# Optimization experiments

Hardware: AMD Instinct MI355X
Metric: run time of the kernel (lower is better)

## Reference

```python
import jax, jax.numpy as jnp
import numpy as np

# Gating config (matches init_kwargs)
N_GROUPS = 4        # n_expert_groups
TOPK_GROUPS = 2     # n_limited_groups
TOPK = 4            # n_activated_experts
ROUTE_SCALE = 1.0


def setup_inputs() -> dict:
    key = jax.random.key(0)
    ks = jax.random.split(key, 8)
    T, D, E, I = 2048, 1024, 16, 512
    s = 0.02  # init scale for sane numerics
    return {
        "x": jax.random.normal(ks[0], (T, D), jnp.float32),
        "gate_w": jax.random.normal(ks[1], (E, D), jnp.float32) * s,
        "w1": jax.random.normal(ks[2], (E, I, D), jnp.float32) * s,
        "w2": jax.random.normal(ks[3], (E, D, I), jnp.float32) * s,
        "w3": jax.random.normal(ks[4], (E, I, D), jnp.float32) * s,
        "ws1": jax.random.normal(ks[5], (I, D), jnp.float32) * s,
        "ws2": jax.random.normal(ks[6], (D, I), jnp.float32) * s,
        "ws3": jax.random.normal(ks[7], (I, D), jnp.float32) * s,
    }


def _gate(x, gate_w):
    # GateDeepSeekV3.forward: softmax scores, group-limited routing, top-k experts.
    T = x.shape[0]
    scores = jax.nn.softmax((x @ gate_w.T).astype(jnp.float32), axis=-1)  # [T, E]
    original_scores = scores
    E = scores.shape[-1]
    # group-limited routing: keep top `TOPK_GROUPS` groups by max score (bias is None)
    s = scores.reshape(T, N_GROUPS, E // N_GROUPS)
    group_scores = s.max(axis=-1)                                  # [T, G]
    _, gidx = jax.lax.top_k(group_scores, TOPK_GROUPS)             # [T, Gk]
    mask = jnp.zeros((T, N_GROUPS), scores.dtype).at[jnp.arange(T)[:, None], gidx].set(1.0)
    s = (s * mask[:, :, None]).reshape(T, E)
    _, indices = jax.lax.top_k(s, TOPK)                            # [T, topk]
    weights = jnp.take_along_axis(original_scores, indices, axis=1) * ROUTE_SCALE
    return weights.astype(x.dtype), indices


def reference(x, gate_w, w1, w2, w3, ws1, ws2, ws3):
    T, D = x.shape
    E = w1.shape[0]
    weights, indices = _gate(x, gate_w)
    # dense [T, E] combine weights (topk indices are unique per token)
    gate_dense = jnp.zeros((T, E), x.dtype).at[jnp.arange(T)[:, None], indices].add(weights)
    # routed experts: y_t = sum_e g[t,e] * W2_e (silu(W1_e x) * (W3_e x))
    h = jax.nn.silu(jnp.einsum('td,eid->tei', x, w1)) * jnp.einsum('td,eid->tei', x, w3)
    y = jnp.einsum('tei,te,edi->td', h, gate_dense, w2)
    # shared expert MLP over all tokens
    z = (jax.nn.silu(x @ ws1.T) * (x @ ws3.T)) @ ws2.T
    return y + z
```

## Files before the change

kernel.cpp:

```cpp
#include <hip/hip_runtime.h>
#include <hip/hip_bf16.h>
#include <math.h>

typedef float v4f __attribute__((ext_vector_type(4)));
typedef short v8s __attribute__((ext_vector_type(8)));

#define T_TOK   2048
#define DDIM    1024
#define NE      16
#define IDIM    512
#define S_ROUTED 8192
#define S_ALL   10240
#define MAXTILE 104

#define OFF_TOPKI    0u
#define OFF_TOPKW    32768u
#define OFF_PART     65536u
#define OFF_CBASE    69632u
#define OFF_SEGOFF   73728u
#define OFF_NTILES   74240u
#define OFF_TROW     74752u
#define OFF_TEND     75776u
#define OFF_TEXP     76800u
#define OFF_SLOTWT   81920u
#define OFF_S2T      114688u
#define OFF_SLOTOF   155648u
#define OFF_W13      (1u<<20)
#define SZ_W13       35651584u
#define OFF_XBF      (OFF_W13 + SZ_W13)
#define OFF_YP       (1u<<20)
#define OFF_H        (43u<<20)
#define OFF_W2B      (56u<<20)

__device__ __forceinline__ unsigned short f2bf(float f) {
    unsigned int u = __float_as_uint(f);
    unsigned int r = (u + 0x7fffu + ((u >> 16) & 1u)) >> 16;
    return (unsigned short)r;
}
__device__ __forceinline__ float bf2f(unsigned short s) {
    return __uint_as_float((unsigned)s << 16);
}

#define GLL16(gp, lp) __builtin_amdgcn_global_load_lds( \
    (__attribute__((address_space(1))) void*)(gp), \
    (__attribute__((address_space(3))) void*)(lp), 16, 0, 0)

__global__ __launch_bounds__(256) void convert_kernel(
    const float* __restrict__ w1, const float* __restrict__ w3, const float* __restrict__ w2,
    const float* __restrict__ s1, const float* __restrict__ s3, const float* __restrict__ s2,
    unsigned short* __restrict__ w13b, unsigned short* __restrict__ w2b)
{
    size_t gid = (size_t)blockIdx.x * 256 + threadIdx.x;
    size_t i4 = gid * 4;
    const float* src;
    unsigned short* dst;
    if (blockIdx.y == 0) {
        int e = (int)(i4 >> 20);
        int rem = (int)(i4 & 1048575u);
        int r2 = rem >> 10, d = rem & 1023;
        int half = (r2 >> 6) & 1;
        int rsrc = ((r2 >> 7) << 6) + (r2 & 63);
        if (e < 16) src = (half ? w3 : w1) + ((size_t)e * 512 + rsrc) * 1024 + d;
        else        src = (half ? s3 : s1) + (size_t)rsrc * 1024 + d;
        dst = w13b + i4;
    } else {
        if (i4 >= 17u * 524288u) return;
        int e = (int)(i4 >> 19);
        int rem = (int)(i4 & 524287u);
        src = (e < 16) ? (w2 + (size_t)e * 524288 + rem) : (s2 + rem);
        dst = w2b + i4;
    }
    float4 v = *(const float4*)src;
    uint2 p;
    p.x = (unsigned)f2bf(v.x) | ((unsigned)f2bf(v.y) << 16);
    p.y = (unsigned)f2bf(v.z) | ((unsigned)f2bf(v.w) << 16);
    *(uint2*)dst = p;
}

__global__ __launch_bounds__(256) void gate_kernel(
    const float* __restrict__ x, const float* __restrict__ gw,
    int* __restrict__ topki, float* __restrict__ topkw,
    unsigned short* __restrict__ xbf)
{
    int t = blockIdx.x;
    int tid = threadIdx.x, lane = tid & 63, wave = tid >> 6;
    const float4* xr = (const float4*)(x + (size_t)t * DDIM);
    float4 xv[4];
#pragma unroll
    for (int j = 0; j < 4; j++) xv[j] = xr[lane + 64 * j];

    __shared__ float sc[NE];
#pragma unroll
    for (int ee = 0; ee < 4; ee++) {
        int e = wave * 4 + ee;
        const float4* wr = (const float4*)(gw + (size_t)e * DDIM);
        float acc = 0.f;
#pragma unroll
        for (int j = 0; j < 4; j++) {
            float4 w = wr[lane + 64 * j];
            acc += xv[j].x * w.x + xv[j].y * w.y + xv[j].z * w.z + xv[j].w * w.w;
        }
#pragma unroll
        for (int off = 32; off; off >>= 1) acc += __shfl_down(acc, off, 64);
        if (lane == 0) sc[e] = acc;
    }
    if (wave == 0) {
#pragma unroll
        for (int j = 0; j < 4; j++) {
            int base = 4 * (lane + 64 * j);
            uint2 p;
            p.x = (unsigned)f2bf(xv[j].x) | ((unsigned)f2bf(xv[j].y) << 16);
            p.y = (unsigned)f2bf(xv[j].z) | ((unsigned)f2bf(xv[j].w) << 16);
            *(uint2*)(xbf + (size_t)t * DDIM + base) = p;
        }
    }
    __syncthreads();
    if (tid == 0) {
        float mx = sc[0];
#pragma unroll
        for (int e = 1; e < NE; e++) mx = fmaxf(mx, sc[e]);
        float sco[NE]; float sum = 0.f;
#pragma unroll
        for (int e = 0; e < NE; e++) { sco[e] = __expf(sc[e] - mx); sum += sco[e]; }
        float inv = 1.f / sum;
#pragma unroll
        for (int e = 0; e < NE; e++) sco[e] *= inv;
        float gs[4];
#pragma unroll
        for (int g = 0; g < 4; g++) {
            float m = sco[4 * g];
            m = fmaxf(m, sco[4 * g + 1]); m = fmaxf(m, sco[4 * g + 2]); m = fmaxf(m, sco[4 * g + 3]);
            gs[g] = m;
        }
        int g0 = 0;
        for (int g = 1; g < 4; g++) if (gs[g] > gs[g0]) g0 = g;
        int g1 = -1;
        for (int g = 0; g < 4; g++) { if (g == g0) continue; if (g1 < 0 || gs[g] > gs[g1]) g1 = g; }
        float ms[NE];
#pragma unroll
        for (int e = 0; e < NE; e++) {
            int g = e >> 2;
            ms[e] = (g == g0 || g == g1) ? sco[e] : 0.0f;
        }
        bool used[NE] = {false};
        for (int k = 0; k < 4; k++) {
            int best = -1;
            for (int e = 0; e < NE; e++) {
                if (used[e]) continue;
                if (best < 0 || ms[e] > ms[best]) best = e;
            }
            used[best] = true;
            topki[t * 4 + k] = best;
            topkw[t * 4 + k] = sco[best];
        }
    }
}

__global__ __launch_bounds__(256) void hist_kernel(
    const int* __restrict__ topki, int* __restrict__ part)
{
    __shared__ int cnt[16];
    int tid = threadIdx.x, b = blockIdx.x;
    if (tid < 16) cnt[tid] = 0;
    __syncthreads();
    int e = topki[b * 256 + tid];
    int lane = tid & 63;
#pragma unroll
    for (int e0 = 0; e0 < 16; e0++) {
        unsigned long long mask = __ballot(e == e0);
        if (lane == 0) atomicAdd(&cnt[e0], __popcll(mask));
    }
    __syncthreads();
    if (tid < 16) part[b * 16 + tid] = cnt[tid];
}

__global__ __launch_bounds__(256) void scan_kernel(
    const int* __restrict__ part, int* __restrict__ cbase, int* __restrict__ segoff,
    int* __restrict__ trow, int* __restrict__ tend, int* __restrict__ texp,
    int* __restrict__ ntp)
{
    int tid = threadIdx.x;
    __shared__ int tot[16];
    __shared__ int so[17];
    if (tid < 16) {
        int s = 0;
        for (int b = 0; b < 32; b++) s += part[b * 16 + tid];
        tot[tid] = s;
    }
    __syncthreads();
    if (tid == 0) {
        int off = 0;
        for (int e = 0; e < 16; e++) { so[e] = off; segoff[e] = off; off += tot[e]; }
        so[16] = off; segoff[16] = off; segoff[17] = off + T_TOK;
        int nt = 0;
        for (int e = 0; e < 17; e++) {
            int n = (e < 16) ? tot[e] : T_TOK;
            int base = (e < 16) ? so[e] : S_ROUTED;
            for (int m = 0; m < n; m += 128) {
                trow[nt] = base + m; tend[nt] = base + n; texp[nt] = e; nt++;
            }
        }
        *ntp = nt;
    }
    __syncthreads();
    if (tid < 16) {
        int run = so[tid];
        for (int b = 0; b < 32; b++) { cbase[b * 16 + tid] = run; run += part[b * 16 + tid]; }
    }
}

__global__ __launch_bounds__(256) void assign_kernel(
    const int* __restrict__ topki, const float* __restrict__ topkw,
    const int* __restrict__ cbase, int* __restrict__ s2t,
    float* __restrict__ slotwt, int* __restrict__ slotof)
{
    int b = blockIdx.x, tid = threadIdx.x;
    int i = b * 256 + tid;
    int e = topki[i];
    int lane = tid & 63, wave = tid >> 6;
    __shared__ int wcnt[4][16];
    int lrank = 0;
#pragma unroll
    for (int e0 = 0; e0 < 16; e0++) {
        unsigned long long mask = __ballot(e == e0);
        if (e == e0) lrank = __popcll(mask & ((1ull << lane) - 1ull));
        if (lane == 0) wcnt[wave][e0] = __popcll(mask);
    }
    __syncthreads();
    int pre = 0;
    for (int w = 0; w < wave; w++) pre += wcnt[w][e];
    int slot = cbase[b * 16 + e] + pre + lrank;
    int t = i >> 2;
    s2t[slot] = t;
    slotwt[slot] = topkw[i];
    slotof[i] = slot;
    if ((i & 3) == 0) s2t[S_ROUTED + t] = t;
}

__global__ __launch_bounds__(256, 2) void gemm1_kernel(
    const unsigned short* __restrict__ w13b, const unsigned short* __restrict__ xbf,
    unsigned short* __restrict__ h, const float* __restrict__ slotwt,
    const int* __restrict__ s2t,
    const int* __restrict__ trow, const int* __restrict__ tend,
    const int* __restrict__ texp, const int* __restrict__ ntp)
{
    int bid = blockIdx.x;
    int tile = bid >> 3, ct = bid & 7;
    if (tile >= *ntp) return;
    int row0 = trow[tile], rend = tend[tile], e = texp[tile];
    int n0 = ct * 64;
    const unsigned short* B = w13b + ((size_t)e << 20) + ((size_t)ct << 17);

    __shared__ __align__(16) short As[2][128 * 64];
    __shared__ __align__(16) short Bs[2][128 * 64];

    int tid = threadIdx.x;
    int lane = tid & 63, wave = tid >> 6;
    int wm = wave & 1, wn = wave >> 1;
    int mq = lane >> 4, nl = lane & 15;
    int rr = lane >> 3, cbl = (lane & 7) ^ rr;

    int tok[4];
#pragma unroll
    for (int j = 0; j < 4; j++)
        tok[j] = s2t[row0 + wave * 32 + j * 8 + rr];

    v4f acc[4][4];
#pragma unroll
    for (int i = 0; i < 4; i++)
#pragma unroll
        for (int j = 0; j < 4; j++) acc[i][j] = (v4f)0.f;

#pragma unroll
    for (int j = 0; j < 4; j++) {
        GLL16(xbf + (size_t)tok[j] * DDIM + cbl * 8, &As[0][wave * 2048 + j * 512]);
        GLL16(B + (size_t)(wave * 32 + j * 8 + rr) * DDIM + cbl * 8, &Bs[0][wave * 2048 + j * 512]);
    }

    for (int ki = 0; ki < 16; ki++) {
        int buf = ki & 1;
        __syncthreads();
        if (ki < 15) {
            int kc = (ki + 1) * 64;
            int nb = buf ^ 1;
#pragma unroll
            for (int j = 0; j < 4; j++) {
                GLL16(xbf + (size_t)tok[j] * DDIM + kc + cbl * 8, &As[nb][wave * 2048 + j * 512]);
                GLL16(B + (size_t)(wave * 32 + j * 8 + rr) * DDIM + kc + cbl * 8, &Bs[nb][wave * 2048 + j * 512]);
            }
        }
#pragma unroll
        for (int ks = 0; ks < 2; ks++) {
            int kb = ks * 4 + mq;
            v8s a[4], b[4];
#pragma unroll
            for (int mi = 0; mi < 4; mi++) {
                int R = wm * 64 + mi * 16 + nl;
                a[mi] = *(const v8s*)(&As[buf][R * 64 + ((kb ^ (nl & 7)) * 8)]);
            }
#pragma unroll
            for (int ni = 0; ni < 4; ni++) {
                int S = (ni >> 1) * 64 + wn * 32 + (ni & 1) * 16 + nl;
                b[ni] = *(const v8s*)(&Bs[buf][S * 64 + ((kb ^ (nl & 7)) * 8)]);
            }
#pragma unroll
            for (int mi = 0; mi < 4; mi++)
#pragma unroll
                for (int ni = 0; ni < 4; ni++)
                    acc[mi][ni] = __builtin_amdgcn_mfma_f32_16x16x32_bf16(a[mi], b[ni], acc[mi][ni], 0, 0, 0);
        }
    }
#pragma unroll
    for (int mi = 0; mi < 4; mi++) {
#pragma unroll
        for (int r = 0; r < 4; r++) {
            int srow = row0 + wm * 64 + mi * 16 + mq * 4 + r;
            if (srow < rend) {
                float g = (srow < S_ROUTED) ? slotwt[srow] : 1.0f;
#pragma unroll
                for (int ni = 0; ni < 2; ni++) {
                    float p1 = acc[mi][ni][r], p3 = acc[mi][ni + 2][r];
                    float sig = 1.f / (1.f + __expf(-p1));
                    h[(size_t)srow * IDIM + n0 + wn * 32 + ni * 16 + nl] = f2bf(p1 * sig * p3 * g);
                }
            }
        }
    }
}

__global__ __launch_bounds__(256, 2) void gemm2_kernel(
    const unsigned short* __restrict__ w2b, const unsigned short* __restrict__ h,
    unsigned short* __restrict__ yp,
    const int* __restrict__ trow, const int* __restrict__ tend,
    const int* __restrict__ texp, const int* __restrict__ ntp)
{
    int bid = blockIdx.x;
    int tile = bid >> 3, ct = bid & 7;
    if (tile >= *ntp) return;
    int row0 = trow[tile], rend = tend[tile], e = texp[tile];
    int n0 = ct * 128;
    const unsigned short* B = w2b + ((size_t)e * DDIM + n0) * IDIM;

    __shared__ __align__(16) short As[2][128 * 64];
    __shared__ __align__(16) short Bs[2][128 * 64];

    int tid = threadIdx.x;
    int lane = tid & 63, wave = tid >> 6;
    int wm = wave & 1, wn = wave >> 1;
    int mq = lane >> 4, nl = lane & 15;
    int rr = lane >> 3, cbl = (lane & 7) ^ rr;

    v4f acc[4][4];
#pragma unroll
    for (int i = 0; i < 4; i++)
#pragma unroll
        for (int j = 0; j < 4; j++) acc[i][j] = (v4f)0.f;

#pragma unroll
    for (int j = 0; j < 4; j++) {
        GLL16(h + (size_t)(row0 + wave * 32 + j * 8 + rr) * IDIM + cbl * 8,
              &As[0][wave * 2048 + j * 512]);
        GLL16(B + (size_t)(wave * 32 + j * 8 + rr) * IDIM + cbl * 8,
              &Bs[0][wave * 2048 + j * 512]);
    }

    for (int ki = 0; ki < 8; ki++) {
        int buf = ki & 1;
        __syncthreads();
        if (ki < 7) {
            int kc = (ki + 1) * 64;
            int nb = buf ^ 1;
#pragma unroll
            for (int j = 0; j < 4; j++) {
                GLL16(h + (size_t)(row0 + wave * 32 + j * 8 + rr) * IDIM + kc + cbl * 8,
                      &As[nb][wave * 2048 + j * 512]);
                GLL16(B + (size_t)(wave * 32 + j * 8 + rr) * IDIM + kc + cbl * 8,
                      &Bs[nb][wave * 2048 + j * 512]);
            }
        }
#pragma unroll
        for (int ks = 0; ks < 2; ks++) {
            int kb = ks * 4 + mq;
            v8s a[4], b[4];
#pragma unroll
            for (int mi = 0; mi < 4; mi++) {
                int R = wm * 64 + mi * 16 + nl;
                a[mi] = *(const v8s*)(&As[buf][R * 64 + ((kb ^ (nl & 7)) * 8)]);
            }
#pragma unroll
            for (int ni = 0; ni < 4; ni++) {
                int S = wn * 64 + ni * 16 + nl;
                b[ni] = *(const v8s*)(&Bs[buf][S * 64 + ((kb ^ (nl & 7)) * 8)]);
            }
#pragma unroll
            for (int mi = 0; mi < 4; mi++)
#pragma unroll
                for (int ni = 0; ni < 4; ni++)
                    acc[mi][ni] = __builtin_amdgcn_mfma_f32_16x16x32_bf16(a[mi], b[ni], acc[mi][ni], 0, 0, 0);
        }
    }
#pragma unroll
    for (int mi = 0; mi < 4; mi++) {
#pragma unroll
        for (int r = 0; r < 4; r++) {
            int srow = row0 + wm * 64 + mi * 16 + mq * 4 + r;
            if (srow < rend) {
                unsigned short* yrow = yp + ((size_t)srow << 10) + n0 + wn * 64 + nl;
#pragma unroll
                for (int ni = 0; ni < 4; ni++)
                    yrow[ni * 16] = f2bf(acc[mi][ni][r]);
            }
        }
    }
}

__global__ __launch_bounds__(256) void combine_kernel(
    const unsigned short* __restrict__ yp, const int* __restrict__ slotof,
    float* __restrict__ out)
{
    int t = blockIdx.x;
    int c = threadIdx.x * 4;
    int s0 = slotof[t * 4 + 0], s1 = slotof[t * 4 + 1];
    int s2 = slotof[t * 4 + 2], s3 = slotof[t * 4 + 3];
    ushort4 v  = *(const ushort4*)(yp + (((size_t)(S_ROUTED + t)) << 10) + c);
    ushort4 a0 = *(const ushort4*)(yp + (((size_t)s0) << 10) + c);
    ushort4 a1 = *(const ushort4*)(yp + (((size_t)s1) << 10) + c);
    ushort4 a2 = *(const ushort4*)(yp + (((size_t)s2) << 10) + c);
    ushort4 a3 = *(const ushort4*)(yp + (((size_t)s3) << 10) + c);
    float4 o;
    o.x = bf2f(v.x) + bf2f(a0.x) + bf2f(a1.x) + bf2f(a2.x) + bf2f(a3.x);
    o.y = bf2f(v.y) + bf2f(a0.y) + bf2f(a1.y) + bf2f(a2.y) + bf2f(a3.y);
    o.z = bf2f(v.z) + bf2f(a0.z) + bf2f(a1.z) + bf2f(a2.z) + bf2f(a3.z);
    o.w = bf2f(v.w) + bf2f(a0.w) + bf2f(a1.w) + bf2f(a2.w) + bf2f(a3.w);
    *(float4*)(out + (((size_t)t) << 10) + c) = o;
}

extern "C" void kernel_launch(void* const* d_in, const int* in_sizes, int n_in,
                              void* d_out, int out_size, void* d_ws, size_t ws_size,
                              hipStream_t stream) {
    const float* x    = (const float*)d_in[0];
    const float* gw   = (const float*)d_in[1];
    const float* w1   = (const float*)d_in[2];
    const float* w2   = (const float*)d_in[3];
    const float* w3   = (const float*)d_in[4];
    const float* wsh1 = (const float*)d_in[5];
    const float* wsh2 = (const float*)d_in[6];
    const float* wsh3 = (const float*)d_in[7];
    float* out = (float*)d_out;

    char* ws = (char*)d_ws;
    int*   topki  = (int*)(ws + OFF_TOPKI);
    float* topkw  = (float*)(ws + OFF_TOPKW);
    int*   part   = (int*)(ws + OFF_PART);
    int*   cbase  = (int*)(ws + OFF_CBASE);
    int*   segoff = (int*)(ws + OFF_SEGOFF);
    int*   ntp    = (int*)(ws + OFF_NTILES);
    int*   trow   = (int*)(ws + OFF_TROW);
    int*   tend   = (int*)(ws + OFF_TEND);
    int*   texp   = (int*)(ws + OFF_TEXP);
    float* slotwt = (float*)(ws + OFF_SLOTWT);
    int*   s2t    = (int*)(ws + OFF_S2T);
    int*   slotof = (int*)(ws + OFF_SLOTOF);
    unsigned short* w13b = (unsigned short*)(ws + OFF_W13);
    unsigned short* xbf  = (unsigned short*)(ws + OFF_XBF);
    unsigned short* yp   = (unsigned short*)(ws + OFF_YP);
    unsigned short* h    = (unsigned short*)(ws + OFF_H);
    unsigned short* w2b  = (unsigned short*)(ws + OFF_W2B);

    convert_kernel<<<dim3(17408, 2), 256, 0, stream>>>(w1, w3, w2, wsh1, wsh3, wsh2,
                                                       w13b, w2b);
    gate_kernel<<<T_TOK, 256, 0, stream>>>(x, gw, topki, topkw, xbf);
    hist_kernel<<<32, 256, 0, stream>>>(topki, part);
    scan_kernel<<<1, 256, 0, stream>>>(part, cbase, segoff, trow, tend, texp, ntp);
    assign_kernel<<<32, 256, 0, stream>>>(topki, topkw, cbase, s2t, slotwt, slotof);
    gemm1_kernel<<<MAXTILE * 8, 256, 0, stream>>>(w13b, xbf, h, slotwt, s2t,
                                                  trow, tend, texp, ntp);
    gemm2_kernel<<<MAXTILE * 8, 256, 0, stream>>>(w2b, h, yp, trow, tend, texp, ntp);
    combine_kernel<<<T_TOK, 256, 0, stream>>>(yp, slotof, out);
}
```

Measured before the change: 247.9 us.

## Fuse fp32-to-bf16 weight conversion into GEMM loads, drop convert kernel

Removes the separate weight conversion pass that wrote bf16 copies of all expert and shared weights. Each GEMM now loads fp32 weight tiles into registers, converts them to bf16 and stores them swizzled into LDS. The LDS tiles go from double to single buffering, with register prefetch of the next B tile, and occupancy is raised to 3 blocks. This avoids one full read and write of the weights, but each GEMM tile re-reads fp32 weights at twice the bytes and loses async LDS double buffering for the activation operand.

```diff
diff --git a/kernel.cpp b/kernel.cpp
--- a/kernel.cpp
+++ b/kernel.cpp
@@ -25,12 +25,9 @@
 #define OFF_SLOTWT   81920u
 #define OFF_S2T      114688u
 #define OFF_SLOTOF   155648u
-#define OFF_W13      (1u<<20)
-#define SZ_W13       35651584u
-#define OFF_XBF      (OFF_W13 + SZ_W13)
-#define OFF_YP       (1u<<20)
-#define OFF_H        (43u<<20)
-#define OFF_W2B      (56u<<20)
+#define OFF_XBF      (1u<<20)
+#define OFF_H        (8u<<20)
+#define OFF_YP       (24u<<20)
 
 __device__ __forceinline__ unsigned short f2bf(float f) {
     unsigned int u = __float_as_uint(f);
@@ -44,38 +41,6 @@
 #define GLL16(gp, lp) __builtin_amdgcn_global_load_lds( \
     (__attribute__((address_space(1))) void*)(gp), \
     (__attribute__((address_space(3))) void*)(lp), 16, 0, 0)
-
-__global__ __launch_bounds__(256) void convert_kernel(
-    const float* __restrict__ w1, const float* __restrict__ w3, const float* __restrict__ w2,
-    const float* __restrict__ s1, const float* __restrict__ s3, const float* __restrict__ s2,
-    unsigned short* __restrict__ w13b, unsigned short* __restrict__ w2b)
-{
-    size_t gid = (size_t)blockIdx.x * 256 + threadIdx.x;
-    size_t i4 = gid * 4;
-    const float* src;
-    unsigned short* dst;
-    if (blockIdx.y == 0) {
-        int e = (int)(i4 >> 20);
-        int rem = (int)(i4 & 1048575u);
-        int r2 = rem >> 10, d = rem & 1023;
-        int half = (r2 >> 6) & 1;
-        int rsrc = ((r2 >> 7) << 6) + (r2 & 63);
-        if (e < 16) src = (half ? w3 : w1) + ((size_t)e * 512 + rsrc) * 1024 + d;
-        else        src = (half ? s3 : s1) + (size_t)rsrc * 1024 + d;
-        dst = w13b + i4;
-    } else {
-        if (i4 >= 17u * 524288u) return;
-        int e = (int)(i4 >> 19);
-        int rem = (int)(i4 & 524287u);
-        src = (e < 16) ? (w2 + (size_t)e * 524288 + rem) : (s2 + rem);
-        dst = w2b + i4;
-    }
-    float4 v = *(const float4*)src;
-    uint2 p;
-    p.x = (unsigned)f2bf(v.x) | ((unsigned)f2bf(v.y) << 16);
-    p.y = (unsigned)f2bf(v.z) | ((unsigned)f2bf(v.w) << 16);
-    *(uint2*)dst = p;
-}
 
 __global__ __launch_bounds__(256) void gate_kernel(
     const float* __restrict__ x, const float* __restrict__ gw,
@@ -237,8 +202,10 @@
     if ((i & 3) == 0) s2t[S_ROUTED + t] = t;
 }
 
-__global__ __launch_bounds__(256, 2) void gemm1_kernel(
-    const unsigned short* __restrict__ w13b, const unsigned short* __restrict__ xbf,
+__global__ __launch_bounds__(256, 3) void gemm1_kernel(
+    const float* __restrict__ w1, const float* __restrict__ w3,
+    const float* __restrict__ s1, const float* __restrict__ s3,
+    const unsigned short* __restrict__ xbf,
     unsigned short* __restrict__ h, const float* __restrict__ slotwt,
     const int* __restrict__ s2t,
     const int* __restrict__ trow, const int* __restrict__ tend,
@@ -249,10 +216,11 @@
     if (tile >= *ntp) return;
     int row0 = trow[tile], rend = tend[tile], e = texp[tile];
     int n0 = ct * 64;
-    const unsigned short* B = w13b + ((size_t)e << 20) + ((size_t)ct << 17);
-
-    __shared__ __align__(16) short As[2][128 * 64];
-    __shared__ __align__(16) short Bs[2][128 * 64];
+    const float* B1 = (e < 16) ? (w1 + (size_t)e * 524288) : s1;
+    const float* B3 = (e < 16) ? (w3 + (size_t)e * 524288) : s3;
+
+    __shared__ __align__(16) short As[128 * 64];
+    __shared__ __align__(16) short Bs[128 * 64];
 
     int tid = threadIdx.x;
     int lane = tid & 63, wave = tid >> 6;
@@ -265,28 +233,51 @@
     for (int j = 0; j < 4; j++)
         tok[j] = s2t[row0 + wave * 32 + j * 8 + rr];
 
+    const float* bsrc[4];
+    int brow[4], bblk[4];
+#pragma unroll
+    for (int j = 0; j < 4; j++) {
+        int u = tid + 256 * j;
+        brow[j] = u >> 3; bblk[j] = u & 7;
+        int half = brow[j] >> 6;
+        const float* base = half ? B3 : B1;
+        bsrc[j] = base + (size_t)(n0 + (brow[j] & 63)) * DDIM + bblk[j] * 8;
+    }
+
     v4f acc[4][4];
 #pragma unroll
     for (int i = 0; i < 4; i++)
 #pragma unroll
         for (int j = 0; j < 4; j++) acc[i][j] = (v4f)0.f;
 
+    float4 br0[4], br1[4];
 #pragma unroll
     for (int j = 0; j < 4; j++) {
-        GLL16(xbf + (size_t)tok[j] * DDIM + cbl * 8, &As[0][wave * 2048 + j * 512]);
-        GLL16(B + (size_t)(wave * 32 + j * 8 + rr) * DDIM + cbl * 8, &Bs[0][wave * 2048 + j * 512]);
+        br0[j] = *(const float4*)(bsrc[j]);
+        br1[j] = *(const float4*)(bsrc[j] + 4);
     }
 
     for (int ki = 0; ki < 16; ki++) {
-        int buf = ki & 1;
+        int kc = ki * 64;
+        __syncthreads();
+#pragma unroll
+        for (int j = 0; j < 4; j++)
+            GLL16(xbf + (size_t)tok[j] * DDIM + kc + cbl * 8, As + wave * 2048 + j * 512);
+#pragma unroll
+        for (int j = 0; j < 4; j++) {
+            uint4 p;
+            p.x = (unsigned)f2bf(br0[j].x) | ((unsigned)f2bf(br0[j].y) << 16);
+            p.y = (unsigned)f2bf(br0[j].z) | ((unsigned)f2bf(br0[j].w) << 16);
+            p.z = (unsigned)f2bf(br1[j].x) | ((unsigned)f2bf(br1[j].y) << 16);
+            p.w = (unsigned)f2bf(br1[j].z) | ((unsigned)f2bf(br1[j].w) << 16);
+            *(uint4*)(Bs + brow[j] * 64 + ((bblk[j] ^ (brow[j] & 7)) * 8)) = p;
+        }
         __syncthreads();
         if (ki < 15) {
-            int kc = (ki + 1) * 64;
-            int nb = buf ^ 1;
 #pragma unroll
             for (int j = 0; j < 4; j++) {
-                GLL16(xbf + (size_t)tok[j] * DDIM + kc + cbl * 8, &As[nb][wave * 2048 + j * 512]);
-                GLL16(B + (size_t)(wave * 32 + j * 8 + rr) * DDIM + kc + cbl * 8, &Bs[nb][wave * 2048 + j * 512]);
+                br0[j] = *(const float4*)(bsrc[j] + kc + 64);
+                br1[j] = *(const float4*)(bsrc[j] + kc + 68);
             }
         }
 #pragma unroll
@@ -296,12 +287,12 @@
 #pragma unroll
             for (int mi = 0; mi < 4; mi++) {
                 int R = wm * 64 + mi * 16 + nl;
-                a[mi] = *(const v8s*)(&As[buf][R * 64 + ((kb ^ (nl & 7)) * 8)]);
+                a[mi] = *(const v8s*)(As + R * 64 + ((kb ^ (nl & 7)) * 8));
             }
 #pragma unroll
             for (int ni = 0; ni < 4; ni++) {
                 int S = (ni >> 1) * 64 + wn * 32 + (ni & 1) * 16 + nl;
-                b[ni] = *(const v8s*)(&Bs[buf][S * 64 + ((kb ^ (nl & 7)) * 8)]);
+                b[ni] = *(const v8s*)(Bs + S * 64 + ((kb ^ (nl & 7)) * 8));
             }
 #pragma unroll
             for (int mi = 0; mi < 4; mi++)
@@ -328,9 +319,9 @@
     }
 }
 
-__global__ __launch_bounds__(256, 2) void gemm2_kernel(
-    const unsigned short* __restrict__ w2b, const unsigned short* __restrict__ h,
-    unsigned short* __restrict__ yp,
+__global__ __launch_bounds__(256, 3) void gemm2_kernel(
+    const float* __restrict__ w2, const float* __restrict__ s2w,
+    const unsigned short* __restrict__ h, unsigned short* __restrict__ yp,
     const int* __restrict__ trow, const int* __restrict__ tend,
     const int* __restrict__ texp, const int* __restrict__ ntp)
 {
@@ -339,10 +330,10 @@
     if (tile >= *ntp) return;
     int row0 = trow[tile], rend = tend[tile], e = texp[tile];
     int n0 = ct * 128;
-    const unsigned short* B = w2b + ((size_t)e * DDIM + n0) * IDIM;
-
-    __shared__ __align__(16) short As[2][128 * 64];
-    __shared__ __align__(16) short Bs[2][128 * 64];
+    const float* B = ((e < 16) ? (w2 + (size_t)e * 524288) : s2w) + (size_t)n0 * IDIM;
+
+    __shared__ __align__(16) short As[128 * 64];
+    __shared__ __align__(16) short Bs[128 * 64];
 
     int tid = threadIdx.x;
     int lane = tid & 63, wave = tid >> 6;
@@ -350,32 +341,50 @@
     int mq = lane >> 4, nl = lane & 15;
     int rr = lane >> 3, cbl = (lane & 7) ^ rr;
 
+    const float* bsrc[4];
+    int brow[4], bblk[4];
+#pragma unroll
+    for (int j = 0; j < 4; j++) {
+        int u = tid + 256 * j;
+        brow[j] = u >> 3; bblk[j] = u & 7;
+        bsrc[j] = B + (size_t)brow[j] * IDIM + bblk[j] * 8;
+    }
+
     v4f acc[4][4];
 #pragma unroll
     for (int i = 0; i < 4; i++)
 #pragma unroll
         for (int j = 0; j < 4; j++) acc[i][j] = (v4f)0.f;
 
+    float4 br0[4], br1[4];
 #pragma unroll
     for (int j = 0; j < 4; j++) {
-        GLL16(h + (size_t)(row0 + wave * 32 + j * 8 + rr) * IDIM + cbl * 8,
-              &As[0][wave * 2048 + j * 512]);
-        GLL16(B + (size_t)(wave * 32 + j * 8 + rr) * IDIM + cbl * 8,
-              &Bs[0][wave * 2048 + j * 512]);
+        br0[j] = *(const float4*)(bsrc[j]);
+        br1[j] = *(const float4*)(bsrc[j] + 4);
     }
 
     for (int ki = 0; ki < 8; ki++) {
-        int buf = ki & 1;
+        int kc = ki * 64;
+        __syncthreads();
+#pragma unroll
+        for (int j = 0; j < 4; j++)
+            GLL16(h + (size_t)(row0 + wave * 32 + j * 8 + rr) * IDIM + kc + cbl * 8,
+                  As + wave * 2048 + j * 512);
+#pragma unroll
+        for (int j = 0; j < 4; j++) {
+            uint4 p;
+            p.x = (unsigned)f2bf(br0[j].x) | ((unsigned)f2bf(br0[j].y) << 16);
+            p.y = (unsigned)f2bf(br0[j].z) | ((unsigned)f2bf(br0[j].w) << 16);
+            p.z = (unsigned)f2bf(br1[j].x) | ((unsigned)f2bf(br1[j].y) << 16);
+            p.w = (unsigned)f2bf(br1[j].z) | ((unsigned)f2bf(br1[j].w) << 16);
+            *(uint4*)(Bs + brow[j] * 64 + ((bblk[j] ^ (brow[j] & 7)) * 8)) = p;
+        }
         __syncthreads();
         if (ki < 7) {
-            int kc = (ki + 1) * 64;
-            int nb = buf ^ 1;
 #pragma unroll
             for (int j = 0; j < 4; j++) {
-                GLL16(h + (size_t)(row0 + wave * 32 + j * 8 + rr) * IDIM + kc + cbl * 8,
-                      &As[nb][wave * 2048 + j * 512]);
-                GLL16(B + (size_t)(wave * 32 + j * 8 + rr) * IDIM + kc + cbl * 8,
-                      &Bs[nb][wave * 2048 + j * 512]);
+                br0[j] = *(const float4*)(bsrc[j] + kc + 64);
+                br1[j] = *(const float4*)(bsrc[j] + kc + 68);
             }
         }
 #pragma unroll
@@ -385,12 +394,12 @@
 #pragma unroll
             for (int mi = 0; mi < 4; mi++) {
                 int R = wm * 64 + mi * 16 + nl;
-                a[mi] = *(const v8s*)(&As[buf][R * 64 + ((kb ^ (nl & 7)) * 8)]);
+                a[mi] = *(const v8s*)(As + R * 64 + ((kb ^ (nl & 7)) * 8));
             }
 #pragma unroll
             for (int ni = 0; ni < 4; ni++) {
                 int S = wn * 64 + ni * 16 + nl;
-                b[ni] = *(const v8s*)(&Bs[buf][S * 64 + ((kb ^ (nl & 7)) * 8)]);
+                b[ni] = *(const v8s*)(Bs + S * 64 + ((kb ^ (nl & 7)) * 8));
             }
 #pragma unroll
             for (int mi = 0; mi < 4; mi++)
@@ -461,20 +470,16 @@
     float* slotwt = (float*)(ws + OFF_SLOTWT);
     int*   s2t    = (int*)(ws + OFF_S2T);
     int*   slotof = (int*)(ws + OFF_SLOTOF);
-    unsigned short* w13b = (unsigned short*)(ws + OFF_W13);
-    unsigned short* xbf  = (unsigned short*)(ws + OFF_XBF);
-    unsigned short* yp   = (unsigned short*)(ws + OFF_YP);
-    unsigned short* h    = (unsigned short*)(ws + OFF_H);
-    unsigned short* w2b  = (unsigned short*)(ws + OFF_W2B);
-
-    convert_kernel<<<dim3(17408, 2), 256, 0, stream>>>(w1, w3, w2, wsh1, wsh3, wsh2,
-                                                       w13b, w2b);
+    unsigned short* xbf = (unsigned short*)(ws + OFF_XBF);
+    unsigned short* h   = (unsigned short*)(ws + OFF_H);
+    unsigned short* yp  = (unsigned short*)(ws + OFF_YP);
+
     gate_kernel<<<T_TOK, 256, 0, stream>>>(x, gw, topki, topkw, xbf);
     hist_kernel<<<32, 256, 0, stream>>>(topki, part);
     scan_kernel<<<1, 256, 0, stream>>>(part, cbase, segoff, trow, tend, texp, ntp);
     assign_kernel<<<32, 256, 0, stream>>>(topki, topkw, cbase, s2t, slotwt, slotof);
-    gemm1_kernel<<<MAXTILE * 8, 256, 0, stream>>>(w13b, xbf, h, slotwt, s2t,
+    gemm1_kernel<<<MAXTILE * 8, 256, 0, stream>>>(w1, w3, wsh1, wsh3, xbf, h, slotwt, s2t,
                                                   trow, tend, texp, ntp);
-    gemm2_kernel<<<MAXTILE * 8, 256, 0, stream>>>(w2b, h, yp, trow, tend, texp, ntp);
+    gemm2_kernel<<<MAXTILE * 8, 256, 0, stream>>>(w2, wsh2, h, yp, trow, tend, texp, ntp);
     combine_kernel<<<T_TOK, 256, 0, stream>>>(yp, slotof, out);
 }
```

After: 228.9 us. -7.7%, faster.
